# Kernel optimization log

Measured on AMD Instinct MI355X. Metric: run time of the kernel, lower is better.

Reference implementation:

```python
import jax, jax.numpy as jnp
import numpy as np

D = 128
H = 4
B = 4096
K = 64
N_USERS = 200000
BISECT_ITERS = 50


def l2norm(x, axis=-1, eps=1e-12):
    n = jnp.linalg.norm(x, axis=axis, keepdims=True)
    return x / jnp.maximum(n, eps)


def entmax_bisect(x, alpha, n_iter=BISECT_ITERS):
    # x, alpha: [B, K, 1]; entmax normalization over the neighbor axis (axis=1)
    # p = max((alpha-1)*x - tau, 0)**(1/(alpha-1)) with tau found by bisection so sum_k p = 1
    am1 = alpha - 1.0            # in (0,1) since alpha = sigmoid(.)+1
    q = 1.0 / am1                # exponent > 1, so p is smooth at 0
    xs = x * am1
    mx = jnp.max(xs, axis=1, keepdims=True)
    tau_lo = mx - 1.0            # f(tau_lo) >= 0
    tau_hi = mx                  # f(tau_hi) <= 0

    def p_of(tau):
        t = jnp.maximum(xs - tau, 0.0)
        safe = jnp.where(t > 0.0, t, 1.0)
        return jnp.where(t > 0.0, safe ** q, 0.0)

    def body(i, carry):
        lo, hi = carry
        mid = 0.5 * (lo + hi)
        f_m = jnp.sum(p_of(mid), axis=1, keepdims=True) - 1.0
        lo = jnp.where(f_m >= 0.0, mid, lo)
        hi = jnp.where(f_m >= 0.0, hi, mid)
        return (lo, hi)

    tau_lo, tau_hi = jax.lax.fori_loop(0, n_iter, body, (tau_lo, tau_hi))
    p = p_of(0.5 * (tau_lo + tau_hi))
    return p / jnp.sum(p, axis=1, keepdims=True)


def batchnorm(x, g, b, eps=1e-5):
    # training-mode BatchNorm1d: batch statistics, biased variance
    m = jnp.mean(x, axis=0)
    v = jnp.mean((x - m) ** 2, axis=0)
    return (x - m) * jax.lax.rsqrt(v + eps) * g + b


def setup_inputs() -> dict:
    key = jax.random.key(0)
    ks = jax.random.split(key, 16)
    s = 0.05
    return {
        'nodes': jax.random.randint(ks[0], (B,), 0, N_USERS),
        'neighbors': jax.random.randint(ks[1], (B, K), 0, N_USERS),
        'u2e': jax.random.normal(ks[2], (N_USERS, D), jnp.float32),
        'att1_w': jax.random.normal(ks[3], (H, 2 * D, D), jnp.float32) * s,
        'att1_b': jnp.zeros((H, D), jnp.float32),
        'att2_w': jax.random.normal(ks[4], (H, D, D // 4), jnp.float32) * s,
        'att2_b': jnp.zeros((H, D // 4), jnp.float32),
        'att3_w': jax.random.normal(ks[5], (H, D // 4, 1), jnp.float32) * s,
        'att3_b': jnp.zeros((H, 1), jnp.float32),
        'lin1_w': jax.random.normal(ks[6], (H, D, 1), jnp.float32) * s,
        'lin1_b': jnp.zeros((H, 1), jnp.float32),
        'gate_w': jax.random.normal(ks[7], (3 * D, D), jnp.float32) * s,
        'gate_b': jnp.zeros((D,), jnp.float32),
        'bn_g': jnp.ones((D,), jnp.float32),
        'bn_b': jnp.zeros((D,), jnp.float32),
        'bn1_g': jnp.ones((D,), jnp.float32),
        'bn1_b': jnp.zeros((D,), jnp.float32),
        'in_w': jax.random.normal(ks[8], (D, D), jnp.float32) * s,
        'in_b': jnp.zeros((D,), jnp.float32),
        'out_w': jax.random.normal(ks[9], (D, D), jnp.float32) * s,
        'out_b': jnp.zeros((D,), jnp.float32),
    }


def reference(nodes, neighbors, u2e, att1_w, att1_b, att2_w, att2_b, att3_w,
              att3_b, lin1_w, lin1_b, gate_w, gate_b, bn_g, bn_b, bn1_g,
              bn1_b, in_w, in_b, out_w, out_b):
    n_heads = att1_w.shape[0]
    e_n = l2norm(u2e[neighbors])                     # [B,K,D] normalized neighbor embeds
    u = u2e[nodes]                                   # [B,D]
    b, k, d = e_n.shape
    feats = []
    for h in range(n_heads):
        u_n = l2norm(u)
        x = jnp.concatenate(
            [e_n, jnp.broadcast_to(u_n[:, None, :], (b, k, d))], axis=-1)
        alpha = jax.nn.sigmoid(e_n @ lin1_w[h] + lin1_b[h]) + 1.0  # [B,K,1]
        sc = jax.nn.selu(x @ att1_w[h] + att1_b[h])
        sc = jax.nn.selu(sc @ att2_w[h] + att2_b[h])
        sc = sc @ att3_w[h] + att3_b[h]                            # [B,K,1]
        att = entmax_bisect(sc, alpha)                             # [B,K,1]
        u = jnp.einsum('bkd,bk->bd', e_n, att[..., 0])             # weighted pool
        feats.append(u)
    att_hist = sum(feats) / n_heads                  # [B,D]
    # GAT_MLP (dropout omitted: eval)
    h1 = batchnorm(att_hist, bn_g, bn_b)
    h1 = jax.nn.selu(h1 @ in_w + in_b)
    h1 = batchnorm(h1, bn1_g, bn1_b)
    neigh = h1 @ out_w + out_b                       # [B,D]
    self_f = u2e[nodes]
    comb = jnp.concatenate([self_f, neigh, self_f * neigh], axis=-1)
    gama = jax.nn.sigmoid(comb @ gate_w + gate_b)
    return gama * self_f + (1.0 - gama) * neigh
```

## Files before the change

kernel.cpp:

```cpp
#include <hip/hip_runtime.h>
#include <stdint.h>

#define NB 4096
#define NK 64
#define ND 128
#define NH 4
#define ES 136
#define ESW (ES/2)
#define FS 130
#define MR 16

typedef __attribute__((ext_vector_type(8))) short bf16x8;
typedef __attribute__((ext_vector_type(4))) float f32x4;

__device__ __forceinline__ float seluf(float x) {
    return 1.0507009873554805f * (x > 0.f ? x : 1.6732632423543772f * (expf(x) - 1.f));
}
__device__ __forceinline__ float sigmoidf_(float x) {
    return 1.f / (1.f + expf(-x));
}
__device__ __forceinline__ uint32_t f2bf2(float a, float b) {
    uint32_t ua = __float_as_uint(a); ua += 0x7fffu + ((ua >> 16) & 1u);
    uint32_t ub = __float_as_uint(b); ub += 0x7fffu + ((ub >> 16) & 1u);
    return (ua >> 16) | (ub & 0xffff0000u);
}
__device__ __forceinline__ uint16_t bf1(float v) {
    uint32_t u = __float_as_uint(v); u += 0x7fffu + ((u >> 16) & 1u);
    return (uint16_t)(u >> 16);
}
__device__ __forceinline__ float bflo(uint32_t v) { return __uint_as_float(v << 16); }
__device__ __forceinline__ float bfhi(uint32_t v) { return __uint_as_float(v & 0xffff0000u); }
__device__ __forceinline__ float bf2f(uint16_t h) { return __uint_as_float(((uint32_t)h) << 16); }

__global__ __launch_bounds__(256)
void k_prep(const float* __restrict__ att1_w, const float* __restrict__ att2_w,
            uint16_t* __restrict__ wt1, uint16_t* __restrict__ wt2)
{
    const int h = blockIdx.x;
    const int t = threadIdx.x;
    {
        int n = t >> 1, kh = t & 1;
        for (int k0 = 0; k0 < 64; ++k0) {
            int k = k0 * 2 + kh;
            float v = att1_w[(size_t)h * 32768 + (size_t)k * ND + n];
            float vo = __shfl_xor(v, 1, 64);
            if (kh == 0)
                ((uint32_t*)wt1)[((size_t)h * ND + n) * 64 + k0] = f2bf2(v, vo);
        }
    }
    {
        int c = t & 31, dh = t >> 5;
        for (int d0 = 0; d0 < 16; ++d0) {
            int d = d0 * 8 + dh;
            float v = att2_w[(size_t)h * 4096 + (size_t)d * 32 + c];
            float vo = __shfl_xor(v, 32, 64);
            if ((dh & 1) == 0)
                ((uint32_t*)wt2)[((size_t)h * 32 + c) * 64 + d0 * 4 + (dh >> 1)] = f2bf2(v, vo);
        }
    }
}

__global__ __launch_bounds__(256, 4)
void k_att(const int* __restrict__ nodes, const int* __restrict__ neighbors,
           const float* __restrict__ u2e,
           const float* __restrict__ att1_w, const float* __restrict__ att1_b,
           const float* __restrict__ att2_b,
           const float* __restrict__ att3_w, const float* __restrict__ att3_b,
           const float* __restrict__ lin1_w, const float* __restrict__ lin1_b,
           const uint16_t* __restrict__ wt1, const uint16_t* __restrict__ wt2,
           float* __restrict__ hist_out,
           float* __restrict__ sums, float* __restrict__ sumsq)
{
    __shared__ alignas(16) uint16_t e_sh[NK * ES];
    __shared__ alignas(16) uint16_t s1_sh[NK * ES];
    __shared__ float u_sh[ND], un_sh[ND], up_sh[ND], lw_sh[ND], hist_sh[ND];
    __shared__ float alpha_sh[NK], sc_sh[NK], att_sh[NK];
    __shared__ float red_sh[256];
    __shared__ float rnorm_sh;

    const int b = blockIdx.x;
    const int t = threadIdx.x;
    const int lane = t & 63;
    const int wave = t >> 6;
    const int lh = lane & 15;
    const int lg = lane >> 4;

    for (int k = wave; k < NK; k += 4) {
        int idx = neighbors[b * NK + k];
        float2 v = ((const float2*)(u2e + (size_t)idx * ND))[lane];
        float ss = v.x * v.x + v.y * v.y;
        #pragma unroll
        for (int m = 1; m < 64; m <<= 1) ss += __shfl_xor(ss, m, 64);
        float r = 1.0f / fmaxf(sqrtf(ss), 1e-12f);
        ((uint32_t*)e_sh)[k * ESW + lane] = f2bf2(v.x * r, v.y * r);
    }
    if (t < ND) {
        u_sh[t] = u2e[(size_t)nodes[b] * ND + t];
        hist_sh[t] = 0.f;
    }
    __syncthreads();

    for (int h = 0; h < NH; ++h) {
        if (wave == 0) {
            float a = u_sh[lane], c = u_sh[lane + 64];
            float ss = a * a + c * c;
            #pragma unroll
            for (int m = 1; m < 64; m <<= 1) ss += __shfl_xor(ss, m, 64);
            if (lane == 0) rnorm_sh = 1.0f / fmaxf(sqrtf(ss), 1e-12f);
        }
        __syncthreads();
        if (t < ND) {
            un_sh[t] = u_sh[t] * rnorm_sh;
            lw_sh[t] = lin1_w[h * ND + t];
        }
        __syncthreads();

        {
            int d = t & 127, half = t >> 7;
            const float* wb = att1_w + (size_t)h * 32768 + (size_t)(ND + half * 64) * ND + d;
            float p = 0.f;
            #pragma unroll 8
            for (int j = 0; j < 64; ++j)
                p += un_sh[half * 64 + j] * wb[j * ND];
            red_sh[t] = p;
        }
        {
            int k = t >> 2, qd = t & 3;
            const uint32_t* er = (const uint32_t*)e_sh + k * ESW + qd * 16;
            const float* lr = lw_sh + qd * 32;
            float ap = 0.f;
            #pragma unroll 8
            for (int j2 = 0; j2 < 16; ++j2) {
                uint32_t v = er[j2];
                ap += bflo(v) * lr[2 * j2] + bfhi(v) * lr[2 * j2 + 1];
            }
            ap += __shfl_xor(ap, 1, 64);
            ap += __shfl_xor(ap, 2, 64);
            if (qd == 0)
                alpha_sh[k] = sigmoidf_(ap + lin1_b[h]) + 1.0f;
        }
        __syncthreads();
        if (t < ND)
            up_sh[t] = red_sh[t] + red_sh[t + 128] + att1_b[h * ND + t];
        __syncthreads();

        {
            const uint16_t* WB = wt1 + ((size_t)h * ND + wave * 32) * ND;
            bf16x8 B[4][2];
            #pragma unroll
            for (int kk = 0; kk < 4; ++kk)
                #pragma unroll
                for (int nt = 0; nt < 2; ++nt)
                    B[kk][nt] = *(const bf16x8*)(WB + (nt * 16 + lh) * ND + kk * 32 + lg * 8);
            f32x4 z = {0.f, 0.f, 0.f, 0.f};
            f32x4 acc[4][2] = {{z, z}, {z, z}, {z, z}, {z, z}};
            #pragma unroll
            for (int mt = 0; mt < 4; ++mt) {
                #pragma unroll
                for (int kk = 0; kk < 4; ++kk) {
                    bf16x8 A = *(const bf16x8*)(e_sh + (mt * 16 + lh) * ES + kk * 32 + lg * 8);
                    acc[mt][0] = __builtin_amdgcn_mfma_f32_16x16x32_bf16(A, B[kk][0], acc[mt][0], 0, 0, 0);
                    acc[mt][1] = __builtin_amdgcn_mfma_f32_16x16x32_bf16(A, B[kk][1], acc[mt][1], 0, 0, 0);
                }
            }
            float up0 = up_sh[wave * 32 + lh];
            float up1 = up_sh[wave * 32 + 16 + lh];
            #pragma unroll
            for (int mt = 0; mt < 4; ++mt)
                #pragma unroll
                for (int nt = 0; nt < 2; ++nt) {
                    float upv = nt ? up1 : up0;
                    #pragma unroll
                    for (int r = 0; r < 4; ++r) {
                        float v = seluf(acc[mt][nt][r] + upv);
                        s1_sh[(mt * 16 + lg * 4 + r) * ES + wave * 32 + nt * 16 + lh] = bf1(v);
                    }
                }
        }
        __syncthreads();

        {
            const uint16_t* WB2 = wt2 + (size_t)h * 32 * ND;
            bf16x8 B2[4][2];
            #pragma unroll
            for (int kk = 0; kk < 4; ++kk)
                #pragma unroll
                for (int nt = 0; nt < 2; ++nt)
                    B2[kk][nt] = *(const bf16x8*)(WB2 + (nt * 16 + lh) * ND + kk * 32 + lg * 8);
            f32x4 z = {0.f, 0.f, 0.f, 0.f};
            f32x4 acc2[2] = {z, z};
            #pragma unroll
            for (int kk = 0; kk < 4; ++kk) {
                bf16x8 A = *(const bf16x8*)(s1_sh + (wave * 16 + lh) * ES + kk * 32 + lg * 8);
                acc2[0] = __builtin_amdgcn_mfma_f32_16x16x32_bf16(A, B2[kk][0], acc2[0], 0, 0, 0);
                acc2[1] = __builtin_amdgcn_mfma_f32_16x16x32_bf16(A, B2[kk][1], acc2[1], 0, 0, 0);
            }
            float w3a = att3_w[h * 32 + lh],      b2a = att2_b[h * 32 + lh];
            float w3b = att3_w[h * 32 + 16 + lh], b2b = att2_b[h * 32 + 16 + lh];
            float b3 = att3_b[h];
            #pragma unroll
            for (int r = 0; r < 4; ++r) {
                float v = seluf(acc2[0][r] + b2a) * w3a + seluf(acc2[1][r] + b2b) * w3b;
                v += __shfl_xor(v, 1, 64);
                v += __shfl_xor(v, 2, 64);
                v += __shfl_xor(v, 4, 64);
                v += __shfl_xor(v, 8, 64);
                if (lh == 0)
                    sc_sh[wave * 16 + lg * 4 + r] = v + b3;
            }
        }
        __syncthreads();

        if (wave == 0) {
            float x   = sc_sh[lane];
            float am1 = alpha_sh[lane] - 1.0f;
            float q   = 1.0f / am1;
            float em1 = q - 1.0f;
            float xs  = x * am1;
            float mx = xs;
            #pragma unroll
            for (int m = 1; m < 64; m <<= 1) mx = fmaxf(mx, __shfl_xor(mx, m, 64));
            float tau = mx - 1.0f;
            for (int it = 0; it < 10; ++it) {
                float tt = xs - tau;
                bool pos = tt > 0.f;
                float lg2 = log2f(pos ? tt : 1.f);
                float p  = pos ? exp2f(q * lg2) : 0.f;
                float dp = pos ? q * exp2f(em1 * lg2) : 0.f;
                float s0 = p, s1 = dp;
                #pragma unroll
                for (int m = 1; m < 64; m <<= 1) {
                    s0 += __shfl_xor(s0, m, 64);
                    s1 += __shfl_xor(s1, m, 64);
                }
                tau += (s0 - 1.0f) / fmaxf(s1, 1e-30f);
                tau = fminf(tau, mx - 1e-6f);
            }
            float tt = xs - tau;
            bool pos = tt > 0.f;
            float p = pos ? exp2f(q * log2f(pos ? tt : 1.f)) : 0.f;
            float s0 = p;
            #pragma unroll
            for (int m = 1; m < 64; m <<= 1) s0 += __shfl_xor(s0, m, 64);
            att_sh[lane] = p / s0;
        }
        __syncthreads();

        {
            int d = t & 127, half = t >> 7;
            const uint16_t* er = e_sh + (half * 32) * ES + d;
            float p = 0.f;
            #pragma unroll 8
            for (int k = 0; k < 32; ++k)
                p += bf2f(er[k * ES]) * att_sh[half * 32 + k];
            red_sh[t] = p;
        }
        __syncthreads();
        if (t < ND) {
            float un = red_sh[t] + red_sh[t + 128];
            u_sh[t] = un;
            hist_sh[t] += un;
        }
        __syncthreads();
    }
    if (t < ND) {
        float hv = hist_sh[t] * 0.25f;
        hist_out[(size_t)b * ND + t] = hv;
        atomicAdd(&sums[t], hv);
        atomicAdd(&sumsq[t], hv * hv);
    }
}

__global__ __launch_bounds__(256)
void k_mlp1(const float* __restrict__ hist,
            const float* __restrict__ sums, const float* __restrict__ sumsq,
            const float* __restrict__ bn_g, const float* __restrict__ bn_b,
            const float* __restrict__ in_w, const float* __restrict__ in_b,
            float* __restrict__ h1out,
            float* __restrict__ sums1, float* __restrict__ sumsq1)
{
    __shared__ float xh[MR * FS];
    int t = threadIdx.x;
    int row0 = blockIdx.x * MR;
    for (int i = t; i < MR * ND; i += 256) {
        int r = i >> 7, d = i & 127;
        float m  = sums[d]  * (1.f / 4096.f);
        float vv = sumsq[d] * (1.f / 4096.f) - m * m;
        float sc = bn_g[d] * rsqrtf(vv + 1e-5f);
        float sh = bn_b[d] - m * sc;
        xh[r * FS + d] = hist[(size_t)(row0 + r) * ND + d] * sc + sh;
    }
    __syncthreads();
    int dg = t & 15, rg = t >> 4;
    int d0 = dg * 8;
    float acc[8] = {};
    float ebuf;
    for (int j = 0; j < ND; ++j) {
        const float* wr = in_w + (size_t)j * ND + d0;
        float4 wa = *(const float4*)wr, wb = *(const float4*)(wr + 4);
        float w[8] = {wa.x, wa.y, wa.z, wa.w, wb.x, wb.y, wb.z, wb.w};
        ebuf = xh[rg * FS + j];
        #pragma unroll
        for (int c = 0; c < 8; ++c) acc[c] += ebuf * w[c];
    }
    float hv[8];
    #pragma unroll
    for (int c = 0; c < 8; ++c) {
        hv[c] = seluf(acc[c] + in_b[d0 + c]);
        h1out[(size_t)(row0 + rg) * ND + d0 + c] = hv[c];
    }
    __syncthreads();
    #pragma unroll
    for (int c = 0; c < 8; ++c) xh[rg * FS + d0 + c] = hv[c];
    __syncthreads();
    if (t < ND) {
        float s = 0.f, q = 0.f;
        #pragma unroll
        for (int r = 0; r < MR; ++r) {
            float v = xh[r * FS + t];
            s += v; q += v * v;
        }
        atomicAdd(&sums1[t], s);
        atomicAdd(&sumsq1[t], q);
    }
}

__global__ __launch_bounds__(256)
void k_final(const float* __restrict__ h1,
             const float* __restrict__ sums1, const float* __restrict__ sumsq1,
             const float* __restrict__ bn1_g, const float* __restrict__ bn1_b,
             const float* __restrict__ out_w, const float* __restrict__ out_b,
             const float* __restrict__ gate_w, const float* __restrict__ gate_b,
             const int* __restrict__ nodes, const float* __restrict__ u2e,
             float* __restrict__ out)
{
    __shared__ float xh[MR * FS];
    __shared__ float sf[MR * FS];
    __shared__ float ng[MR * FS];
    int t = threadIdx.x;
    int row0 = blockIdx.x * MR;
    for (int i = t; i < MR * ND; i += 256) {
        int r = i >> 7, d = i & 127;
        float m  = sums1[d]  * (1.f / 4096.f);
        float vv = sumsq1[d] * (1.f / 4096.f) - m * m;
        float sc = bn1_g[d] * rsqrtf(vv + 1e-5f);
        float sh = bn1_b[d] - m * sc;
        xh[r * FS + d] = h1[(size_t)(row0 + r) * ND + d] * sc + sh;
        sf[r * FS + d] = u2e[(size_t)nodes[row0 + r] * ND + d];
    }
    __syncthreads();
    int dg = t & 15, rg = t >> 4;
    int d0 = dg * 8;
    {
        float acc[8] = {};
        for (int j = 0; j < ND; ++j) {
            const float* wr = out_w + (size_t)j * ND + d0;
            float4 wa = *(const float4*)wr, wb = *(const float4*)(wr + 4);
            float w[8] = {wa.x, wa.y, wa.z, wa.w, wb.x, wb.y, wb.z, wb.w};
            float e0 = xh[rg * FS + j];
            #pragma unroll
            for (int c = 0; c < 8; ++c) acc[c] += e0 * w[c];
        }
        #pragma unroll
        for (int c = 0; c < 8; ++c)
            ng[rg * FS + d0 + c] = acc[c] + out_b[d0 + c];
    }
    __syncthreads();
    {
        float acc[8] = {};
        for (int j = 0; j < ND; ++j) {
            const float* g0 = gate_w + (size_t)j * ND + d0;
            const float* g1 = gate_w + (size_t)(ND + j) * ND + d0;
            const float* g2 = gate_w + (size_t)(2 * ND + j) * ND + d0;
            float4 a0 = *(const float4*)g0, b0 = *(const float4*)(g0 + 4);
            float4 a1 = *(const float4*)g1, b1 = *(const float4*)(g1 + 4);
            float4 a2 = *(const float4*)g2, b2 = *(const float4*)(g2 + 4);
            float w0[8] = {a0.x, a0.y, a0.z, a0.w, b0.x, b0.y, b0.z, b0.w};
            float w1[8] = {a1.x, a1.y, a1.z, a1.w, b1.x, b1.y, b1.z, b1.w};
            float w2[8] = {a2.x, a2.y, a2.z, a2.w, b2.x, b2.y, b2.z, b2.w};
            float s = sf[rg * FS + j];
            float n = ng[rg * FS + j];
            float p = s * n;
            #pragma unroll
            for (int c = 0; c < 8; ++c)
                acc[c] += s * w0[c] + n * w1[c] + p * w2[c];
        }
        #pragma unroll
        for (int c = 0; c < 8; ++c) {
            int d = d0 + c;
            float gama = sigmoidf_(acc[c] + gate_b[d]);
            float s = sf[rg * FS + d];
            float n = ng[rg * FS + d];
            out[(size_t)(row0 + rg) * ND + d] = gama * s + (1.f - gama) * n;
        }
    }
}

extern "C" void kernel_launch(void* const* d_in, const int* in_sizes, int n_in,
                              void* d_out, int out_size, void* d_ws, size_t ws_size,
                              hipStream_t stream)
{
    const int*   nodes     = (const int*)d_in[0];
    const int*   neighbors = (const int*)d_in[1];
    const float* u2e       = (const float*)d_in[2];
    const float* att1_w    = (const float*)d_in[3];
    const float* att1_b    = (const float*)d_in[4];
    const float* att2_w    = (const float*)d_in[5];
    const float* att2_b    = (const float*)d_in[6];
    const float* att3_w    = (const float*)d_in[7];
    const float* att3_b    = (const float*)d_in[8];
    const float* lin1_w    = (const float*)d_in[9];
    const float* lin1_b    = (const float*)d_in[10];
    const float* gate_w    = (const float*)d_in[11];
    const float* gate_b    = (const float*)d_in[12];
    const float* bn_g      = (const float*)d_in[13];
    const float* bn_b      = (const float*)d_in[14];
    const float* bn1_g     = (const float*)d_in[15];
    const float* bn1_b     = (const float*)d_in[16];
    const float* in_w      = (const float*)d_in[17];
    const float* in_b      = (const float*)d_in[18];
    const float* out_w     = (const float*)d_in[19];
    const float* out_b     = (const float*)d_in[20];
    float* out = (float*)d_out;

    float* ws     = (float*)d_ws;
    float* g_hist = ws;
    float* h1     = ws + (size_t)NB * ND;
    float* st     = ws + (size_t)2 * NB * ND;
    uint16_t* wt1 = (uint16_t*)(ws + (size_t)2 * NB * ND + 512);
    uint16_t* wt2 = wt1 + (size_t)NH * ND * ND;

    (void)hipMemsetAsync(st, 0, 512 * sizeof(float), stream);

    k_prep<<<NH, 256, 0, stream>>>(att1_w, att2_w, wt1, wt2);
    k_att<<<NB, 256, 0, stream>>>(nodes, neighbors, u2e,
                                  att1_w, att1_b, att2_b,
                                  att3_w, att3_b, lin1_w, lin1_b,
                                  wt1, wt2,
                                  g_hist, st, st + 128);
    k_mlp1<<<NB / MR, 256, 0, stream>>>(g_hist, st, st + 128, bn_g, bn_b,
                                        in_w, in_b, h1, st + 256, st + 384);
    k_final<<<NB / MR, 256, 0, stream>>>(h1, st + 256, st + 384, bn1_g, bn1_b,
                                         out_w, out_b, gate_w, gate_b,
                                         nodes, u2e, out);
}
```

Measured before the change: 630.4 us.

## Use fast math intrinsics, cut Newton iterations, repartition pooling and MLP kernels

Result: faster. 559.0 us (-11.3%).

```diff
diff --git a/kernel.cpp b/kernel.cpp
--- a/kernel.cpp
+++ b/kernel.cpp
@@ -8,16 +8,17 @@
 #define ES 136
 #define ESW (ES/2)
 #define FS 130
-#define MR 16
+#define MR 8
 
 typedef __attribute__((ext_vector_type(8))) short bf16x8;
 typedef __attribute__((ext_vector_type(4))) float f32x4;
 
 __device__ __forceinline__ float seluf(float x) {
-    return 1.0507009873554805f * (x > 0.f ? x : 1.6732632423543772f * (expf(x) - 1.f));
+    float e = 1.6732632423543772f * (__expf(x) - 1.f);
+    return 1.0507009873554805f * (x > 0.f ? x : e);
 }
 __device__ __forceinline__ float sigmoidf_(float x) {
-    return 1.f / (1.f + expf(-x));
+    return __fdividef(1.f, 1.f + __expf(-x));
 }
 __device__ __forceinline__ uint32_t f2bf2(float a, float b) {
     uint32_t ua = __float_as_uint(a); ua += 0x7fffu + ((ua >> 16) & 1u);
@@ -36,11 +37,12 @@
 void k_prep(const float* __restrict__ att1_w, const float* __restrict__ att2_w,
             uint16_t* __restrict__ wt1, uint16_t* __restrict__ wt2)
 {
-    const int h = blockIdx.x;
+    const int h = blockIdx.x >> 2;
+    const int q = blockIdx.x & 3;
     const int t = threadIdx.x;
     {
         int n = t >> 1, kh = t & 1;
-        for (int k0 = 0; k0 < 64; ++k0) {
+        for (int k0 = q * 16; k0 < q * 16 + 16; ++k0) {
             int k = k0 * 2 + kh;
             float v = att1_w[(size_t)h * 32768 + (size_t)k * ND + n];
             float vo = __shfl_xor(v, 1, 64);
@@ -50,7 +52,7 @@
     }
     {
         int c = t & 31, dh = t >> 5;
-        for (int d0 = 0; d0 < 16; ++d0) {
+        for (int d0 = q * 4; d0 < q * 4 + 4; ++d0) {
             int d = d0 * 8 + dh;
             float v = att2_w[(size_t)h * 4096 + (size_t)d * 32 + c];
             float vo = __shfl_xor(v, 32, 64);
@@ -75,7 +77,7 @@
     __shared__ alignas(16) uint16_t s1_sh[NK * ES];
     __shared__ float u_sh[ND], un_sh[ND], up_sh[ND], lw_sh[ND], hist_sh[ND];
     __shared__ float alpha_sh[NK], sc_sh[NK], att_sh[NK];
-    __shared__ float red_sh[256];
+    __shared__ float red_sh[512];
     __shared__ float rnorm_sh;
 
     const int b = blockIdx.x;
@@ -221,43 +223,48 @@
             #pragma unroll
             for (int m = 1; m < 64; m <<= 1) mx = fmaxf(mx, __shfl_xor(mx, m, 64));
             float tau = mx - 1.0f;
-            for (int it = 0; it < 10; ++it) {
+            for (int it = 0; it < 8; ++it) {
                 float tt = xs - tau;
                 bool pos = tt > 0.f;
-                float lg2 = log2f(pos ? tt : 1.f);
-                float p  = pos ? exp2f(q * lg2) : 0.f;
-                float dp = pos ? q * exp2f(em1 * lg2) : 0.f;
+                float lgn = __logf(pos ? tt : 1.f);
+                float p  = pos ? __expf(q * lgn) : 0.f;
+                float dp = pos ? q * __expf(em1 * lgn) : 0.f;
                 float s0 = p, s1 = dp;
                 #pragma unroll
                 for (int m = 1; m < 64; m <<= 1) {
                     s0 += __shfl_xor(s0, m, 64);
                     s1 += __shfl_xor(s1, m, 64);
                 }
-                tau += (s0 - 1.0f) / fmaxf(s1, 1e-30f);
+                tau += __fdividef(s0 - 1.0f, fmaxf(s1, 1e-30f));
                 tau = fminf(tau, mx - 1e-6f);
             }
             float tt = xs - tau;
             bool pos = tt > 0.f;
-            float p = pos ? exp2f(q * log2f(pos ? tt : 1.f)) : 0.f;
+            float p = pos ? __expf(q * __logf(pos ? tt : 1.f)) : 0.f;
             float s0 = p;
             #pragma unroll
             for (int m = 1; m < 64; m <<= 1) s0 += __shfl_xor(s0, m, 64);
-            att_sh[lane] = p / s0;
+            att_sh[lane] = __fdividef(p, s0);
         }
         __syncthreads();
 
         {
-            int d = t & 127, half = t >> 7;
-            const uint16_t* er = e_sh + (half * 32) * ES + d;
-            float p = 0.f;
+            int d2 = t & 63, qk = t >> 6;
+            const uint32_t* E = (const uint32_t*)e_sh;
+            float px = 0.f, py = 0.f;
             #pragma unroll 8
-            for (int k = 0; k < 32; ++k)
-                p += bf2f(er[k * ES]) * att_sh[half * 32 + k];
-            red_sh[t] = p;
+            for (int k = qk * 16; k < qk * 16 + 16; ++k) {
+                uint32_t v = E[k * ESW + d2];
+                float a = att_sh[k];
+                px += bflo(v) * a;
+                py += bfhi(v) * a;
+            }
+            red_sh[qk * 128 + d2 * 2]     = px;
+            red_sh[qk * 128 + d2 * 2 + 1] = py;
         }
         __syncthreads();
         if (t < ND) {
-            float un = red_sh[t] + red_sh[t + 128];
+            float un = red_sh[t] + red_sh[128 + t] + red_sh[256 + t] + red_sh[384 + t];
             u_sh[t] = un;
             hist_sh[t] += un;
         }
@@ -291,27 +298,24 @@
         xh[r * FS + d] = hist[(size_t)(row0 + r) * ND + d] * sc + sh;
     }
     __syncthreads();
-    int dg = t & 15, rg = t >> 4;
-    int d0 = dg * 8;
-    float acc[8] = {};
-    float ebuf;
+    int dg = t & 31, rg = t >> 5;
+    int d0 = dg * 4;
+    float acc[4] = {};
     for (int j = 0; j < ND; ++j) {
-        const float* wr = in_w + (size_t)j * ND + d0;
-        float4 wa = *(const float4*)wr, wb = *(const float4*)(wr + 4);
-        float w[8] = {wa.x, wa.y, wa.z, wa.w, wb.x, wb.y, wb.z, wb.w};
-        ebuf = xh[rg * FS + j];
-        #pragma unroll
-        for (int c = 0; c < 8; ++c) acc[c] += ebuf * w[c];
-    }
-    float hv[8];
+        float4 wa = *(const float4*)(in_w + (size_t)j * ND + d0);
+        float e = xh[rg * FS + j];
+        acc[0] += e * wa.x; acc[1] += e * wa.y;
+        acc[2] += e * wa.z; acc[3] += e * wa.w;
+    }
+    float hv[4];
     #pragma unroll
-    for (int c = 0; c < 8; ++c) {
+    for (int c = 0; c < 4; ++c) {
         hv[c] = seluf(acc[c] + in_b[d0 + c]);
         h1out[(size_t)(row0 + rg) * ND + d0 + c] = hv[c];
     }
     __syncthreads();
     #pragma unroll
-    for (int c = 0; c < 8; ++c) xh[rg * FS + d0 + c] = hv[c];
+    for (int c = 0; c < 4; ++c) xh[rg * FS + d0 + c] = hv[c];
     __syncthreads();
     if (t < ND) {
         float s = 0.f, q = 0.f;
@@ -349,44 +353,37 @@
         sf[r * FS + d] = u2e[(size_t)nodes[row0 + r] * ND + d];
     }
     __syncthreads();
-    int dg = t & 15, rg = t >> 4;
-    int d0 = dg * 8;
+    int dg = t & 31, rg = t >> 5;
+    int d0 = dg * 4;
     {
-        float acc[8] = {};
+        float acc[4] = {};
         for (int j = 0; j < ND; ++j) {
-            const float* wr = out_w + (size_t)j * ND + d0;
-            float4 wa = *(const float4*)wr, wb = *(const float4*)(wr + 4);
-            float w[8] = {wa.x, wa.y, wa.z, wa.w, wb.x, wb.y, wb.z, wb.w};
-            float e0 = xh[rg * FS + j];
-            #pragma unroll
-            for (int c = 0; c < 8; ++c) acc[c] += e0 * w[c];
+            float4 wa = *(const float4*)(out_w + (size_t)j * ND + d0);
+            float e = xh[rg * FS + j];
+            acc[0] += e * wa.x; acc[1] += e * wa.y;
+            acc[2] += e * wa.z; acc[3] += e * wa.w;
         }
         #pragma unroll
-        for (int c = 0; c < 8; ++c)
+        for (int c = 0; c < 4; ++c)
             ng[rg * FS + d0 + c] = acc[c] + out_b[d0 + c];
     }
     __syncthreads();
     {
-        float acc[8] = {};
+        float acc[4] = {};
         for (int j = 0; j < ND; ++j) {
-            const float* g0 = gate_w + (size_t)j * ND + d0;
-            const float* g1 = gate_w + (size_t)(ND + j) * ND + d0;
-            const float* g2 = gate_w + (size_t)(2 * ND + j) * ND + d0;
-            float4 a0 = *(const float4*)g0, b0 = *(const float4*)(g0 + 4);
-            float4 a1 = *(const float4*)g1, b1 = *(const float4*)(g1 + 4);
-            float4 a2 = *(const float4*)g2, b2 = *(const float4*)(g2 + 4);
-            float w0[8] = {a0.x, a0.y, a0.z, a0.w, b0.x, b0.y, b0.z, b0.w};
-            float w1[8] = {a1.x, a1.y, a1.z, a1.w, b1.x, b1.y, b1.z, b1.w};
-            float w2[8] = {a2.x, a2.y, a2.z, a2.w, b2.x, b2.y, b2.z, b2.w};
+            float4 w0 = *(const float4*)(gate_w + (size_t)j * ND + d0);
+            float4 w1 = *(const float4*)(gate_w + (size_t)(ND + j) * ND + d0);
+            float4 w2 = *(const float4*)(gate_w + (size_t)(2 * ND + j) * ND + d0);
             float s = sf[rg * FS + j];
             float n = ng[rg * FS + j];
             float p = s * n;
-            #pragma unroll
-            for (int c = 0; c < 8; ++c)
-                acc[c] += s * w0[c] + n * w1[c] + p * w2[c];
+            acc[0] += s * w0.x + n * w1.x + p * w2.x;
+            acc[1] += s * w0.y + n * w1.y + p * w2.y;
+            acc[2] += s * w0.z + n * w1.z + p * w2.z;
+            acc[3] += s * w0.w + n * w1.w + p * w2.w;
         }
         #pragma unroll
-        for (int c = 0; c < 8; ++c) {
+        for (int c = 0; c < 4; ++c) {
             int d = d0 + c;
             float gama = sigmoidf_(acc[c] + gate_b[d]);
             float s = sf[rg * FS + d];
@@ -432,7 +429,7 @@
 
     (void)hipMemsetAsync(st, 0, 512 * sizeof(float), stream);
 
-    k_prep<<<NH, 256, 0, stream>>>(att1_w, att2_w, wt1, wt2);
+    k_prep<<<16, 256, 0, stream>>>(att1_w, att2_w, wt1, wt2);
     k_att<<<NB, 256, 0, stream>>>(nodes, neighbors, u2e,
                                   att1_w, att1_b, att2_b,
                                   att3_w, att3_b, lin1_w, lin1_b,
```
